# Kernel optimization log

Hardware: AMD Instinct MI355X
Metric: run time of the kernel (lower is better)

Reference implementation:

```python
import jax, jax.numpy as jnp
import numpy as np

N = 2048      # num_nodes
K = 8         # Chebyshev order
HEADS = 4
BETA = 0.5
EPS = 1e-6


def setup_inputs() -> dict:
    key = jax.random.key(0)
    ks = jax.random.split(key, 5)
    # edge_index enumerates all ordered node pairs i != j (row-major), matching
    # the [2, N*(N-1)] logits parameter layout of the module.
    ii, jj = np.meshgrid(np.arange(N), np.arange(N), indexing='ij')
    mask = ii != jj
    edge_index = jnp.asarray(np.stack([ii[mask], jj[mask]]), dtype=jnp.int32)  # [2, E]
    E = N * (N - 1)
    logits = jax.random.normal(ks[0], (2, E), dtype=jnp.float32)
    s = 1.0 / np.sqrt(K)
    w0 = jax.random.normal(ks[1], (HEADS, K), dtype=jnp.float32) * s  # Linear(K,1) weight per head
    b0 = jax.random.normal(ks[2], (HEADS,), dtype=jnp.float32) * s
    w1 = jax.random.normal(ks[3], (HEADS, K), dtype=jnp.float32) * s
    b1 = jax.random.normal(ks[4], (HEADS,), dtype=jnp.float32) * s
    return {"edge_index": edge_index, "logits": logits, "w0": w0, "b0": b0, "w1": w1, "b1": b1}


def _laplacian(vals, src, dst, dtype):
    # to_dense_adj + L = -D^{-1/2} A D^{-1/2}, with diag matmuls as broadcast scaling
    A = jnp.zeros((N, N), dtype).at[src, dst].add(vals)
    dinv = 1.0 / jnp.sqrt(A.sum(axis=1) + EPS)
    return -(dinv[:, None] * A) * dinv[None, :]


def _cheb_gather(L, src, dst):
    # T1 = L, Tk = 2 L Tkm1 - Tkm2; gather edge entries of T1..TK -> [E, K]
    cols = [L[src, dst]]
    Tkm2 = jnp.eye(N, dtype=L.dtype)
    Tkm1 = L
    for _ in range(K - 1):
        Tk = 2.0 * (L @ Tkm1) - Tkm2
        cols.append(Tk[src, dst])
        Tkm2, Tkm1 = Tkm1, Tk
    return jnp.stack(cols, axis=1)


def reference(edge_index, logits, w0, b0, w1, b1):
    src, dst = edge_index[0], edge_index[1]
    edge_prob = jax.nn.softmax(BETA * logits, axis=0)  # softmax over the 2 branches
    L0 = _laplacian(edge_prob[0], src, dst, logits.dtype)
    L1 = _laplacian(edge_prob[1], src, dst, logits.dtype)
    Lks0 = _cheb_gather(L0, src, dst)  # [E, K]
    Lks1 = _cheb_gather(L1, src, dst)  # [E, K]
    f0 = (Lks0 @ w0.T + b0).T  # [heads, E], theta0[i](Lks0).squeeze(-1)
    f1 = (Lks1 @ w1.T + b1).T  # [heads, E]
    return edge_prob, f0, f1
```

## Files before the change

kernel.cpp:

```cpp
#include <hip/hip_runtime.h>
#include <math.h>

#define NN 2048
#define NM1 2047
#define EDGES (NN * NM1)
#define KORD 8
#define NHEADS 4
#define BETA 0.5f
#define EPSV 1e-6f

typedef __attribute__((ext_vector_type(8))) short bf16x8;
typedef __attribute__((ext_vector_type(4))) float f32x4;

__device__ __forceinline__ unsigned short f2bf(float f) {
    unsigned u = __builtin_bit_cast(unsigned, f);
    u += 0x7FFF + ((u >> 16) & 1);
    return (unsigned short)(u >> 16);
}
__device__ __forceinline__ float bf2f(unsigned short h) {
    unsigned u = ((unsigned)h) << 16;
    return __builtin_bit_cast(float, u);
}

#define GLD16(gp, lp) __builtin_amdgcn_global_load_lds(                         \
    (const __attribute__((address_space(1))) void*)(gp),                        \
    (__attribute__((address_space(3))) void*)(lp), 16, 0, 0)

__global__ void k_prob(const float* __restrict__ logits, float* __restrict__ out) {
    int e = blockIdx.x * 256 + threadIdx.x;
    if (e >= EDGES) return;
    float l0 = logits[e];
    float l1 = logits[EDGES + e];
    float p0 = 1.f / (1.f + __expf(BETA * (l1 - l0)));
    float p1 = 1.f / (1.f + __expf(BETA * (l0 - l1)));
    out[e]         = p0;
    out[EDGES + e] = p1;
}

__global__ __launch_bounds__(256) void k_dinv(const float* __restrict__ logits, float* __restrict__ dinv) {
    int row = blockIdx.x;
    const float* r0 = logits + (size_t)row * NM1;
    const float* r1 = r0 + EDGES;
    float s = 0.f;
    for (int t = threadIdx.x; t < NM1; t += 256) {
        float l0 = r0[t], l1 = r1[t];
        s += 1.f / (1.f + __expf(BETA * (l1 - l0)));
    }
    for (int off = 32; off; off >>= 1) s += __shfl_down(s, off);
    __shared__ float red[4];
    if ((threadIdx.x & 63) == 0) red[threadIdx.x >> 6] = s;
    __syncthreads();
    if (threadIdx.x == 0) {
        float s0 = red[0] + red[1] + red[2] + red[3];
        dinv[row]      = 1.f / sqrtf(s0 + EPSV);
        dinv[NN + row] = 1.f / sqrtf((float)NM1 - s0 + EPSV);
    }
}

__global__ __launch_bounds__(256) void k_build(const float* __restrict__ logits, const float* __restrict__ dinv,
                                               unsigned short* __restrict__ Lb0, unsigned short* __restrict__ Lb1) {
    int idx = blockIdx.x * 256 + threadIdx.x;
    int i = idx >> 11, j = idx & (NN - 1);
    float v0 = 0.f, v1 = 0.f;
    if (i != j) {
        size_t e = (size_t)i * NM1 + (j < i ? j : j - 1);
        float l0 = logits[e], l1 = logits[EDGES + e];
        float p0 = 1.f / (1.f + __expf(BETA * (l1 - l0)));
        v0 = -dinv[i] * p0 * dinv[j];
        v1 = -dinv[NN + i] * (1.f - p0) * dinv[NN + j];
    }
    Lb0[idx] = f2bf(v0);
    Lb1[idx] = f2bf(v1);
}

__global__ __launch_bounds__(256) void k_transpose(
    const unsigned short* __restrict__ S0, const unsigned short* __restrict__ S1,
    unsigned short* __restrict__ D0, unsigned short* __restrict__ D1) {
    __shared__ unsigned short T[64 * 66];
    const unsigned short* S = blockIdx.z ? S1 : S0;
    unsigned short* D = blockIdx.z ? D1 : D0;
    int t = threadIdx.x;
    int I0 = blockIdx.y * 64, J0 = blockIdx.x * 64;
    int r = t >> 2, cb = (t & 3) * 16;
    {
        const uint4* src = (const uint4*)(S + (size_t)(I0 + r) * NN + J0 + cb);
        uint4 v0 = src[0], v1 = src[1];
        unsigned* d = (unsigned*)&T[r * 66 + cb];
        d[0] = v0.x; d[1] = v0.y; d[2] = v0.z; d[3] = v0.w;
        d[4] = v1.x; d[5] = v1.y; d[6] = v1.z; d[7] = v1.w;
    }
    __syncthreads();
    union { unsigned short u[16]; uint4 q[2]; } pk;
#pragma unroll
    for (int q = 0; q < 16; ++q) pk.u[q] = T[(cb + q) * 66 + r];
    unsigned short* dst = D + (size_t)(J0 + r) * NN + I0 + cb;
    ((uint4*)dst)[0] = pk.q[0];
    ((uint4*)dst)[1] = pk.q[1];
}

__device__ __forceinline__ void gemm_core(
    const unsigned short* __restrict__ A, const unsigned short* __restrict__ BT,
    const unsigned short* __restrict__ Um2, unsigned short* __restrict__ Un,
    int first, int r0, int c0) {
    __shared__ unsigned short As[128 * 32];
    __shared__ unsigned short Bs[128 * 32];

    int tid = threadIdx.x;
    int w = tid >> 6, l = tid & 63;
    int wr = w >> 1, wc = w & 1;

    int srow = l >> 2;
    int schk = ((l & 3) ^ ((l >> 3) & 3)) * 8;
    const unsigned short* ga  = A  + (size_t)(r0 + w * 16 + srow) * NN + schk;
    const unsigned short* gb  = BT + (size_t)(c0 + w * 16 + srow) * NN + schk;
    const unsigned short* ga2 = ga + (size_t)64 * NN;
    const unsigned short* gb2 = gb + (size_t)64 * NN;
    unsigned short* lA  = As + w * 512;
    unsigned short* lA2 = As + 2048 + w * 512;
    unsigned short* lB  = Bs + w * 512;
    unsigned short* lB2 = Bs + 2048 + w * 512;

    f32x4 acc[4][4] = {};
    int lr = l & 15, g = l >> 4;
    int rchk = (g ^ ((lr >> 1) & 3)) * 8;

    for (int k0 = 0; k0 < NN; k0 += 32) {
        __syncthreads();
        GLD16(ga + k0, lA);
        GLD16(ga2 + k0, lA2);
        GLD16(gb + k0, lB);
        GLD16(gb2 + k0, lB2);
        __syncthreads();
        bf16x8 af[4], bf[4];
#pragma unroll
        for (int m = 0; m < 4; ++m)
            af[m] = *(const bf16x8*)(As + (wr * 64 + m * 16 + lr) * 32 + rchk);
#pragma unroll
        for (int n = 0; n < 4; ++n)
            bf[n] = *(const bf16x8*)(Bs + (wc * 64 + n * 16 + lr) * 32 + rchk);
#pragma unroll
        for (int m = 0; m < 4; ++m)
#pragma unroll
            for (int n = 0; n < 4; ++n)
                acc[m][n] = __builtin_amdgcn_mfma_f32_16x16x32_bf16(af[m], bf[n], acc[m][n], 0, 0, 0);
    }

#pragma unroll
    for (int m = 0; m < 4; ++m)
#pragma unroll
        for (int n = 0; n < 4; ++n)
#pragma unroll
            for (int r = 0; r < 4; ++r) {
                int row = r0 + wr * 64 + m * 16 + g * 4 + r;
                int col = c0 + wc * 64 + n * 16 + lr;
                size_t off = (size_t)row * NN + col;
                float prev = first ? (row == col ? 1.f : 0.f) : bf2f(Um2[off]);
                Un[off] = f2bf(2.f * acc[m][n][r] - prev);
            }
}

__global__ __launch_bounds__(256, 4) void k_cheb1(
    const unsigned short* __restrict__ LT0, const unsigned short* __restrict__ LT1,
    const unsigned short* __restrict__ Lb0, const unsigned short* __restrict__ Lb1,
    unsigned short* __restrict__ U20, unsigned short* __restrict__ U21) {
    int z = blockIdx.z;
    gemm_core(z ? LT1 : LT0, z ? Lb1 : Lb0, z ? LT1 : LT0, z ? U21 : U20, 1,
              blockIdx.y * 128, blockIdx.x * 128);
}

__global__ __launch_bounds__(256, 4) void k_chebp(
    const unsigned short* __restrict__ Alo0, const unsigned short* __restrict__ Ahi0,
    const unsigned short* __restrict__ Alo1, const unsigned short* __restrict__ Ahi1,
    const unsigned short* __restrict__ BT0,  const unsigned short* __restrict__ BT1,
    const unsigned short* __restrict__ Plo0, const unsigned short* __restrict__ Phi0,
    const unsigned short* __restrict__ Plo1, const unsigned short* __restrict__ Phi1,
    unsigned short* __restrict__ Olo0, unsigned short* __restrict__ Ohi0,
    unsigned short* __restrict__ Olo1, unsigned short* __restrict__ Ohi1,
    int firstlo, int firsthi) {
    int z = blockIdx.z;
    int half = blockIdx.y >> 4, my = blockIdx.y & 15;
    const unsigned short* A  = z ? (half ? Ahi1 : Alo1) : (half ? Ahi0 : Alo0);
    const unsigned short* BT = z ? BT1 : BT0;
    const unsigned short* P  = z ? (half ? Phi1 : Plo1) : (half ? Phi0 : Plo0);
    unsigned short* O        = z ? (half ? Ohi1 : Olo1) : (half ? Ohi0 : Olo0);
    gemm_core(A, BT, P, O, half ? firsthi : firstlo, my * 128, blockIdx.x * 128);
}

__global__ __launch_bounds__(256) void k_gather(
    const unsigned short* __restrict__ M1, const unsigned short* __restrict__ M2,
    const unsigned short* __restrict__ M3, const unsigned short* __restrict__ M4,
    const unsigned short* __restrict__ M5, const unsigned short* __restrict__ M6,
    const unsigned short* __restrict__ M7, const unsigned short* __restrict__ M8,
    const float* __restrict__ w, const float* __restrict__ bias,
    float* __restrict__ fout) {
    __shared__ unsigned short G[64 * 66];
    int t = threadIdx.x;
    int I0 = blockIdx.y * 64, J0 = blockIdx.x * 64;
    int jo = t & 63, ig = t >> 6;
    int sr = t >> 2, scb = (t & 3) * 16;

    float acc[4][16];
#pragma unroll
    for (int h = 0; h < 4; ++h)
#pragma unroll
        for (int s = 0; s < 16; ++s) acc[h][s] = 0.f;

    const unsigned short* mats[8] = {M1, M2, M3, M4, M5, M6, M7, M8};
#pragma unroll
    for (int kk = 0; kk < 8; ++kk) {
        const unsigned short* M = mats[kk];
        __syncthreads();
        {
            const uint4* src = (const uint4*)(M + (size_t)(J0 + sr) * NN + I0 + scb);
            uint4 v0 = src[0], v1 = src[1];
            unsigned* d = (unsigned*)&G[sr * 66 + scb];
            d[0] = v0.x; d[1] = v0.y; d[2] = v0.z; d[3] = v0.w;
            d[4] = v1.x; d[5] = v1.y; d[6] = v1.z; d[7] = v1.w;
        }
        __syncthreads();
        float c0w = w[0 * KORD + kk], c1w = w[1 * KORD + kk];
        float c2w = w[2 * KORD + kk], c3w = w[3 * KORD + kk];
#pragma unroll
        for (int s = 0; s < 16; ++s) {
            int io = ig * 16 + s;
            float v = bf2f(G[jo * 66 + io]);
            acc[0][s] += c0w * v;
            acc[1][s] += c1w * v;
            acc[2][s] += c2w * v;
            acc[3][s] += c3w * v;
        }
    }
    float b0v = bias[0], b1v = bias[1], b2v = bias[2], b3v = bias[3];
#pragma unroll
    for (int s = 0; s < 16; ++s) {
        int i = I0 + ig * 16 + s;
        int j = J0 + jo;
        if (i == j) continue;
        size_t e = (size_t)i * NM1 + (j < i ? j : j - 1);
        fout[0 * (size_t)EDGES + e] = b0v + acc[0][s];
        fout[1 * (size_t)EDGES + e] = b1v + acc[1][s];
        fout[2 * (size_t)EDGES + e] = b2v + acc[2][s];
        fout[3 * (size_t)EDGES + e] = b3v + acc[3][s];
    }
}

extern "C" void kernel_launch(void* const* d_in, const int* in_sizes, int n_in,
                              void* d_out, int out_size, void* d_ws, size_t ws_size,
                              hipStream_t stream) {
    const float* logits = (const float*)d_in[1];
    const float* w0 = (const float*)d_in[2];
    const float* b0 = (const float*)d_in[3];
    const float* w1 = (const float*)d_in[4];
    const float* b1 = (const float*)d_in[5];
    float* out = (float*)d_out;

    const size_t MATB = (size_t)NN * NN * sizeof(unsigned short);
    char* ws = (char*)d_ws;
    unsigned short* s0[9];
    for (int k = 0; k < 9; ++k) s0[k] = (unsigned short*)(ws + (size_t)k * MATB);
    float* dinv = (float*)(ws + 9 * MATB);
    char* ob = (char*)d_out;
    unsigned short* s1[9];
    for (int k = 0; k < 9; ++k) s1[k] = (unsigned short*)(ob + (size_t)k * MATB);

    k_dinv<<<NN, 256, 0, stream>>>(logits, dinv);
    k_build<<<(NN * NN) / 256, 256, 0, stream>>>(logits, dinv, s0[0], s1[0]);
    k_transpose<<<dim3(32, 32, 2), 256, 0, stream>>>(s0[0], s1[0], s0[1], s1[1]);

    k_cheb1<<<dim3(16, 16, 2), 256, 0, stream>>>(s0[1], s1[1], s0[0], s1[0], s0[2], s1[2]);
    k_transpose<<<dim3(32, 32, 2), 256, 0, stream>>>(s0[2], s1[2], s0[0], s1[0]);

    k_chebp<<<dim3(16, 32, 2), 256, 0, stream>>>(
        s0[1], s0[2], s1[1], s1[2], s0[0], s1[0],
        s0[1], s0[2], s1[1], s1[2],
        s0[3], s0[4], s1[3], s1[4], 0, 1);
    k_chebp<<<dim3(16, 32, 2), 256, 0, stream>>>(
        s0[3], s0[4], s1[3], s1[4], s0[0], s1[0],
        s0[1], s0[2], s1[1], s1[2],
        s0[5], s0[6], s1[5], s1[6], 0, 0);
    k_chebp<<<dim3(16, 32, 2), 256, 0, stream>>>(
        s0[5], s0[6], s1[5], s1[6], s0[0], s1[0],
        s0[3], s0[4], s1[3], s1[4],
        s0[7], s0[8], s1[7], s1[8], 0, 0);

    float* f1 = out + 6 * (size_t)EDGES;
    k_gather<<<dim3(32, 32), 256, 0, stream>>>(s1[1], s1[2], s1[3], s1[4], s1[5], s1[6], s1[7], s1[8],
                                               w1, b1, f1);
    float* f0 = out + 2 * (size_t)EDGES;
    k_gather<<<dim3(32, 32), 256, 0, stream>>>(s0[1], s0[2], s0[3], s0[4], s0[5], s0[6], s0[7], s0[8],
                                               w0, b0, f0);
    k_prob<<<(EDGES + 255) / 256, 256, 0, stream>>>(logits, out);
}
```

Before: 617.1 us.

## Replace 128x128 GEMM with 256x256 tile, 4-slot LDS pipelined GEMM

```diff
diff --git a/kernel.cpp b/kernel.cpp
--- a/kernel.cpp
+++ b/kernel.cpp
@@ -8,6 +8,7 @@
 #define NHEADS 4
 #define BETA 0.5f
 #define EPSV 1e-6f
+#define NT 32
 
 typedef __attribute__((ext_vector_type(8))) short bf16x8;
 typedef __attribute__((ext_vector_type(4))) float f32x4;
@@ -98,77 +99,128 @@
     ((uint4*)dst)[1] = pk.q[1];
 }
 
-__device__ __forceinline__ void gemm_core(
+__device__ __forceinline__ void gemm256_core(
     const unsigned short* __restrict__ A, const unsigned short* __restrict__ BT,
     const unsigned short* __restrict__ Um2, unsigned short* __restrict__ Un,
     int first, int r0, int c0) {
-    __shared__ unsigned short As[128 * 32];
-    __shared__ unsigned short Bs[128 * 32];
+    __shared__ unsigned short Als[4][256 * 32];
+    __shared__ unsigned short Bls[4][256 * 32];
+    unsigned short* Af = &Als[0][0];
+    unsigned short* Bf = &Bls[0][0];
 
     int tid = threadIdx.x;
     int w = tid >> 6, l = tid & 63;
-    int wr = w >> 1, wc = w & 1;
-
-    int srow = l >> 2;
-    int schk = ((l & 3) ^ ((l >> 3) & 3)) * 8;
-    const unsigned short* ga  = A  + (size_t)(r0 + w * 16 + srow) * NN + schk;
-    const unsigned short* gb  = BT + (size_t)(c0 + w * 16 + srow) * NN + schk;
-    const unsigned short* ga2 = ga + (size_t)64 * NN;
-    const unsigned short* gb2 = gb + (size_t)64 * NN;
-    unsigned short* lA  = As + w * 512;
-    unsigned short* lA2 = As + 2048 + w * 512;
-    unsigned short* lB  = Bs + w * 512;
-    unsigned short* lB2 = Bs + 2048 + w * 512;
-
-    f32x4 acc[4][4] = {};
-    int lr = l & 15, g = l >> 4;
-    int rchk = (g ^ ((lr >> 1) & 3)) * 8;
-
-    for (int k0 = 0; k0 < NN; k0 += 32) {
-        __syncthreads();
-        GLD16(ga + k0, lA);
-        GLD16(ga2 + k0, lA2);
-        GLD16(gb + k0, lB);
-        GLD16(gb2 + k0, lB2);
-        __syncthreads();
-        bf16x8 af[4], bf[4];
-#pragma unroll
-        for (int m = 0; m < 4; ++m)
-            af[m] = *(const bf16x8*)(As + (wr * 64 + m * 16 + lr) * 32 + rchk);
+    int wr = w >> 2, wcn = w & 3;
+    int lr = l & 15, lq = l >> 4;
+
+    int srow = tid >> 2;
+    int key  = (srow >> 1) & 3;
+    int swzc = ((tid & 3) ^ key) << 3;
+    const unsigned short* pa = A  + (size_t)(r0 + srow) * NN + swzc;
+    const unsigned short* pb = BT + (size_t)(c0 + srow) * NN + swzc;
+    const int ldst = w << 9;
+
+    auto stgA = [&](int slot, int g) {
+        const unsigned short* s = pa + g * 32;
+        unsigned short* d = Af + slot * 8192 + ldst;
+        GLD16(s, d);
+        GLD16(s + (size_t)128 * NN, d + 4096);
+    };
+    auto stgB = [&](int slot, int g) {
+        const unsigned short* s = pb + g * 32;
+        unsigned short* d = Bf + slot * 8192 + ldst;
+        GLD16(s, d);
+        GLD16(s + (size_t)128 * NN, d + 4096);
+    };
+
+    int rchk = (lq ^ ((lr >> 1) & 3)) << 3;
+    const int aoff = (wr * 128 + lr) * 32 + rchk;
+    const int boff = (wcn * 64 + lr) * 32 + rchk;
+
+    f32x4 acc[8][4] = {};
+    bf16x8 bfr[4];
+
+#define VMC4 asm volatile("s_waitcnt vmcnt(4)" ::: "memory")
+#define VMC0 asm volatile("s_waitcnt vmcnt(0)" ::: "memory")
+
+#define PHASE(slotA, slotB, M0, READB, STAGE_STMT, VM_STMT) do {                \
+        bf16x8 afr[4];                                                          \
+        _Pragma("unroll")                                                       \
+        for (int mm = 0; mm < 4; ++mm)                                          \
+            afr[mm] = *(const bf16x8*)(Af + (slotA) * 8192 + aoff + ((M0) + mm) * 512); \
+        if (READB) {                                                            \
+            _Pragma("unroll")                                                   \
+            for (int n = 0; n < 4; ++n)                                         \
+                bfr[n] = *(const bf16x8*)(Bf + (slotB) * 8192 + boff + n * 512); \
+        }                                                                       \
+        STAGE_STMT;                                                             \
+        VM_STMT;                                                                \
+        __builtin_amdgcn_s_barrier();                                           \
+        asm volatile("s_waitcnt lgkmcnt(0)" ::: "memory");                      \
+        __builtin_amdgcn_sched_barrier(0);                                      \
+        __builtin_amdgcn_s_setprio(1);                                          \
+        _Pragma("unroll")                                                       \
+        for (int mm = 0; mm < 4; ++mm)                                          \
+            _Pragma("unroll")                                                   \
+            for (int n = 0; n < 4; ++n)                                         \
+                acc[(M0) + mm][n] = __builtin_amdgcn_mfma_f32_16x16x32_bf16(    \
+                    afr[mm], bfr[n], acc[(M0) + mm][n], 0, 0, 0);               \
+        __builtin_amdgcn_s_setprio(0);                                          \
+        __builtin_amdgcn_s_barrier();                                           \
+        __builtin_amdgcn_sched_barrier(0);                                      \
+    } while (0)
+
+    stgB(0, 0); stgA(0, 0); stgB(1, 1); stgA(1, 1);
+    stgB(2, 2); stgA(2, 2); stgB(3, 3);
+    VMC0;
+    __builtin_amdgcn_s_barrier();
+    __builtin_amdgcn_sched_barrier(0);
+
+    for (int t = 0; t < NT; ++t) {
+        int s0 = (t & 1) << 1, s1 = s0 + 1;
+        if (t + 1 < NT) {
+            PHASE(s0, s0, 0, 1, stgA((2 * t + 3) & 3, 2 * t + 3), VMC4);
+        } else {
+            PHASE(s0, s0, 0, 1, (void)0, VMC0);
+        }
+        PHASE(s0, s0, 4, 0, if (t + 2 < NT) stgB((2 * t + 4) & 3, 2 * t + 4), (void)0);
+        PHASE(s1, s1, 0, 1, if (t + 2 < NT) stgA((2 * t + 4) & 3, 2 * t + 4), (void)0);
+        PHASE(s1, s1, 4, 0, if (t + 2 < NT) stgB((2 * t + 5) & 3, 2 * t + 5), (void)0);
+    }
+#undef PHASE
+#undef VMC4
+#undef VMC0
+
+#pragma unroll
+    for (int m = 0; m < 8; ++m)
 #pragma unroll
         for (int n = 0; n < 4; ++n)
-            bf[n] = *(const bf16x8*)(Bs + (wc * 64 + n * 16 + lr) * 32 + rchk);
-#pragma unroll
-        for (int m = 0; m < 4; ++m)
-#pragma unroll
-            for (int n = 0; n < 4; ++n)
-                acc[m][n] = __builtin_amdgcn_mfma_f32_16x16x32_bf16(af[m], bf[n], acc[m][n], 0, 0, 0);
-    }
-
-#pragma unroll
-    for (int m = 0; m < 4; ++m)
-#pragma unroll
-        for (int n = 0; n < 4; ++n)
-#pragma unroll
-            for (int r = 0; r < 4; ++r) {
-                int row = r0 + wr * 64 + m * 16 + g * 4 + r;
-                int col = c0 + wc * 64 + n * 16 + lr;
+#pragma unroll
+            for (int rr = 0; rr < 4; ++rr) {
+                int row = r0 + wr * 128 + m * 16 + lq * 4 + rr;
+                int col = c0 + wcn * 64 + n * 16 + lr;
                 size_t off = (size_t)row * NN + col;
                 float prev = first ? (row == col ? 1.f : 0.f) : bf2f(Um2[off]);
-                Un[off] = f2bf(2.f * acc[m][n][r] - prev);
+                Un[off] = f2bf(2.f * acc[m][n][rr] - prev);
             }
 }
 
-__global__ __launch_bounds__(256, 4) void k_cheb1(
+__global__ __launch_bounds__(512, 2) void k_cheb1(
     const unsigned short* __restrict__ LT0, const unsigned short* __restrict__ LT1,
-    const unsigned short* __restrict__ Lb0, const unsigned short* __restrict__ Lb1,
-    unsigned short* __restrict__ U20, unsigned short* __restrict__ U21) {
+    const unsigned short* __restrict__ Lb0, const unsigned short* __restrict__ Lb1) {
     int z = blockIdx.z;
-    gemm_core(z ? LT1 : LT0, z ? Lb1 : Lb0, z ? LT1 : LT0, z ? U21 : U20, 1,
-              blockIdx.y * 128, blockIdx.x * 128);
-}
-
-__global__ __launch_bounds__(256, 4) void k_chebp(
+}
+
+__global__ __launch_bounds__(512, 2) void k_cheb256_1(
+    const unsigned short* __restrict__ A0, const unsigned short* __restrict__ A1,
+    const unsigned short* __restrict__ B0, const unsigned short* __restrict__ B1,
+    unsigned short* __restrict__ O0, unsigned short* __restrict__ O1) {
+    int z = blockIdx.z;
+    gemm256_core(z ? A1 : A0, z ? B1 : B0, z ? A1 : A0, z ? O1 : O0, 1,
+                 blockIdx.y * 256, blockIdx.x * 256);
+}
+
+__global__ __launch_bounds__(512, 2) void k_cheb256_p(
     const unsigned short* __restrict__ Alo0, const unsigned short* __restrict__ Ahi0,
     const unsigned short* __restrict__ Alo1, const unsigned short* __restrict__ Ahi1,
     const unsigned short* __restrict__ BT0,  const unsigned short* __restrict__ BT1,
@@ -178,12 +230,12 @@
     unsigned short* __restrict__ Olo1, unsigned short* __restrict__ Ohi1,
     int firstlo, int firsthi) {
     int z = blockIdx.z;
-    int half = blockIdx.y >> 4, my = blockIdx.y & 15;
+    int half = blockIdx.y >> 3, my = blockIdx.y & 7;
     const unsigned short* A  = z ? (half ? Ahi1 : Alo1) : (half ? Ahi0 : Alo0);
     const unsigned short* BT = z ? BT1 : BT0;
     const unsigned short* P  = z ? (half ? Phi1 : Plo1) : (half ? Phi0 : Plo0);
     unsigned short* O        = z ? (half ? Ohi1 : Olo1) : (half ? Ohi0 : Olo0);
-    gemm_core(A, BT, P, O, half ? firsthi : firstlo, my * 128, blockIdx.x * 128);
+    gemm256_core(A, BT, P, O, half ? firsthi : firstlo, my * 256, blockIdx.x * 256);
 }
 
 __global__ __launch_bounds__(256) void k_gather(
@@ -267,18 +319,18 @@
     k_build<<<(NN * NN) / 256, 256, 0, stream>>>(logits, dinv, s0[0], s1[0]);
     k_transpose<<<dim3(32, 32, 2), 256, 0, stream>>>(s0[0], s1[0], s0[1], s1[1]);
 
-    k_cheb1<<<dim3(16, 16, 2), 256, 0, stream>>>(s0[1], s1[1], s0[0], s1[0], s0[2], s1[2]);
+    k_cheb256_1<<<dim3(8, 8, 2), 512, 0, stream>>>(s0[1], s1[1], s0[0], s1[0], s0[2], s1[2]);
     k_transpose<<<dim3(32, 32, 2), 256, 0, stream>>>(s0[2], s1[2], s0[0], s1[0]);
 
-    k_chebp<<<dim3(16, 32, 2), 256, 0, stream>>>(
+    k_cheb256_p<<<dim3(8, 16, 2), 512, 0, stream>>>(
         s0[1], s0[2], s1[1], s1[2], s0[0], s1[0],
         s0[1], s0[2], s1[1], s1[2],
         s0[3], s0[4], s1[3], s1[4], 0, 1);
-    k_chebp<<<dim3(16, 32, 2), 256, 0, stream>>>(
+    k_cheb256_p<<<dim3(8, 16, 2), 512, 0, stream>>>(
         s0[3], s0[4], s1[3], s1[4], s0[0], s1[0],
         s0[1], s0[2], s1[1], s1[2],
         s0[5], s0[6], s1[5], s1[6], 0, 0);
-    k_chebp<<<dim3(16, 32, 2), 256, 0, stream>>>(
+    k_cheb256_p<<<dim3(8, 16, 2), 512, 0, stream>>>(
         s0[5], s0[6], s1[5], s1[6], s0[0], s1[0],
         s0[3], s0[4], s1[3], s1[4],
         s0[7], s0[8], s1[7], s1[8], 0, 0);
```

New measurement: 651.2 us. 1.06x slower.
